# Kernel optimization log

Hardware: AMD Instinct MI355X
Metric: run time of the kernel (lower is better)

The kernel has to match this reference:

```python
import jax, jax.numpy as jnp
import numpy as np

BIT_WEIGHTS = jnp.asarray(1 << np.arange(7, -1, -1), dtype=jnp.uint8)  # big-endian bit order


def _packbits_last(bits):
    """Pack 0/1 uint8 bits along the last axis into uint8 bytes (big bitorder).
    bits: [..., N] uint8 in {0,1}. Returns [..., ceil(N/8)] uint8."""
    n = bits.shape[-1]
    pad = (-n) % 8
    if pad:
        bits = jnp.pad(bits, [(0, 0)] * (bits.ndim - 1) + [(0, pad)])
    bits = bits.reshape(bits.shape[:-1] + ((n + pad) // 8, 8))
    # weighted sum over the 8-bit group; max value 255 fits in uint8
    return jnp.sum(bits * BIT_WEIGHTS, axis=-1, dtype=jnp.uint8)


def setup_inputs() -> dict:
    key = jax.random.key(0)
    kx, _ = jax.random.split(key)
    x = jax.random.normal(kx, (4096, 8192), dtype=jnp.float32)  # normalized FP32 input
    depth = jnp.asarray([-0.67, 0.0, 0.67], dtype=jnp.float32)  # TH_DEPTH3 thresholds
    return {"x": x, "depth": depth}


def reference(x, depth):
    # x: [b, i] float32; depth: [D] thresholds
    # compare -> [b, D, i] bits, then pack along last axis -> [b, D, ceil(i/8)] uint8
    bits = (x[:, None, :] > depth[None, :, None]).astype(jnp.uint8)
    return _packbits_last(bits)
```

## Files before the change

kernel.cpp:

```cpp
#include <hip/hip_runtime.h>


typedef float nfloat4 __attribute__((ext_vector_type(4)));
typedef int   nint4   __attribute__((ext_vector_type(4)));

constexpr int ROWS = 4096;
constexpr int COLS = 8192;
constexpr int BYTES_PER_ROW = COLS / 8;
constexpr int TOTAL = ROWS * BYTES_PER_ROW;
constexpr int BLOCK = 256;
constexpr int GROUPS = TOTAL / 4;
constexpr int GRID = GROUPS / BLOCK;

__global__ __launch_bounds__(BLOCK) void binarize_pack_kernel(
    const float* __restrict__ x,
    const float* __restrict__ depth,
    int* __restrict__ out) {
    const int g = blockIdx.x * BLOCK + threadIdx.x;

    const float d0 = depth[0];
    const float d1 = depth[1];
    const float d2 = depth[2];

    const nfloat4* xv = reinterpret_cast<const nfloat4*>(x) + (size_t)g * 8;
    nfloat4 r[8];
#pragma unroll
    for (int i = 0; i < 8; ++i) r[i] = __builtin_nontemporal_load(xv + i);

    float v[32];
#pragma unroll
    for (int i = 0; i < 8; ++i) {
        v[4 * i + 0] = r[i].x;
        v[4 * i + 1] = r[i].y;
        v[4 * i + 2] = r[i].z;
        v[4 * i + 3] = r[i].w;
    }

    nint4 o0, o1, o2;
#pragma unroll
    for (int b = 0; b < 4; ++b) {
        unsigned p0 = 0, p1 = 0, p2 = 0;
#pragma unroll
        for (int k = 0; k < 8; ++k) {
            const unsigned w = 1u << (7 - k);
            const float val = v[8 * b + k];
            p0 |= (val > d0) ? w : 0u;
            p1 |= (val > d1) ? w : 0u;
            p2 |= (val > d2) ? w : 0u;
        }
        o0[b] = (int)p0;
        o1[b] = (int)p1;
        o2[b] = (int)p2;
    }

    const int byte0 = g * 4;
    const int row = byte0 >> 10;
    const int col = byte0 & 1023;
    int* o = out + (size_t)row * (3 * BYTES_PER_ROW) + col;
    __builtin_nontemporal_store(o0, reinterpret_cast<nint4*>(o + 0 * BYTES_PER_ROW));
    __builtin_nontemporal_store(o1, reinterpret_cast<nint4*>(o + 1 * BYTES_PER_ROW));
    __builtin_nontemporal_store(o2, reinterpret_cast<nint4*>(o + 2 * BYTES_PER_ROW));
}

extern "C" void kernel_launch(void* const* d_in, const int* in_sizes, int n_in,
                              void* d_out, int out_size, void* d_ws, size_t ws_size,
                              hipStream_t stream) {
    const float* x = (const float*)d_in[0];
    const float* depth = (const float*)d_in[1];
    int* out = (int*)d_out;

    binarize_pack_kernel<<<GRID, BLOCK, 0, stream>>>(x, depth, out);
}
```

Before: 233.4 us.

## Stage row loads through swizzled LDS for coalesced global reads

```diff
diff --git a/kernel.cpp b/kernel.cpp
--- a/kernel.cpp
+++ b/kernel.cpp
@@ -7,33 +7,42 @@
 constexpr int ROWS = 4096;
 constexpr int COLS = 8192;
 constexpr int BYTES_PER_ROW = COLS / 8;
-constexpr int TOTAL = ROWS * BYTES_PER_ROW;
 constexpr int BLOCK = 256;
-constexpr int GROUPS = TOTAL / 4;
-constexpr int GRID = GROUPS / BLOCK;
+constexpr int VEC_PER_ROW = COLS / 4;
+
+__device__ __forceinline__ int swz(int p) {
+    return p ^ ((p >> 3) & 7);
+}
 
 __global__ __launch_bounds__(BLOCK) void binarize_pack_kernel(
     const float* __restrict__ x,
     const float* __restrict__ depth,
     int* __restrict__ out) {
-    const int g = blockIdx.x * BLOCK + threadIdx.x;
+    __shared__ nfloat4 lds[VEC_PER_ROW];
+
+    const int row = blockIdx.x;
+    const int tid = threadIdx.x;
 
     const float d0 = depth[0];
     const float d1 = depth[1];
     const float d2 = depth[2];
 
-    const nfloat4* xv = reinterpret_cast<const nfloat4*>(x) + (size_t)g * 8;
-    nfloat4 r[8];
+    const nfloat4* xrow = reinterpret_cast<const nfloat4*>(x) + (size_t)row * VEC_PER_ROW;
 #pragma unroll
-    for (int i = 0; i < 8; ++i) r[i] = __builtin_nontemporal_load(xv + i);
+    for (int j = 0; j < 8; ++j) {
+        const int p = j * BLOCK + tid;
+        lds[swz(p)] = __builtin_nontemporal_load(xrow + p);
+    }
+    __syncthreads();
 
     float v[32];
 #pragma unroll
-    for (int i = 0; i < 8; ++i) {
-        v[4 * i + 0] = r[i].x;
-        v[4 * i + 1] = r[i].y;
-        v[4 * i + 2] = r[i].z;
-        v[4 * i + 3] = r[i].w;
+    for (int j = 0; j < 8; ++j) {
+        const nfloat4 q = lds[swz(8 * tid + j)];
+        v[4 * j + 0] = q.x;
+        v[4 * j + 1] = q.y;
+        v[4 * j + 2] = q.z;
+        v[4 * j + 3] = q.w;
     }
 
     nint4 o0, o1, o2;
@@ -53,13 +62,10 @@
         o2[b] = (int)p2;
     }
 
-    const int byte0 = g * 4;
-    const int row = byte0 >> 10;
-    const int col = byte0 & 1023;
-    int* o = out + (size_t)row * (3 * BYTES_PER_ROW) + col;
-    __builtin_nontemporal_store(o0, reinterpret_cast<nint4*>(o + 0 * BYTES_PER_ROW));
-    __builtin_nontemporal_store(o1, reinterpret_cast<nint4*>(o + 1 * BYTES_PER_ROW));
-    __builtin_nontemporal_store(o2, reinterpret_cast<nint4*>(o + 2 * BYTES_PER_ROW));
+    int* orow = out + (size_t)row * (3 * BYTES_PER_ROW);
+    __builtin_nontemporal_store(o0, reinterpret_cast<nint4*>(orow + 0 * BYTES_PER_ROW) + tid);
+    __builtin_nontemporal_store(o1, reinterpret_cast<nint4*>(orow + 1 * BYTES_PER_ROW) + tid);
+    __builtin_nontemporal_store(o2, reinterpret_cast<nint4*>(orow + 2 * BYTES_PER_ROW) + tid);
 }
 
 extern "C" void kernel_launch(void* const* d_in, const int* in_sizes, int n_in,
@@ -69,5 +75,5 @@
     const float* depth = (const float*)d_in[1];
     int* out = (int*)d_out;
 
-    binarize_pack_kernel<<<GRID, BLOCK, 0, stream>>>(x, depth, out);
+    binarize_pack_kernel<<<ROWS, BLOCK, 0, stream>>>(x, depth, out);
 }
```

Measured after the change: 194.0 us. 1.2x faster.
